# Kernel tuning notes

Measured on AMD Instinct MI355X. Metric: run time of the kernel, lower is better.

Reference implementation:

```python
import jax, jax.numpy as jnp
import numpy as np

HID = 1024; INTER = 2048; NSTATE = 16; KCONV = 4; DTRANK = 64
NHEADS = 16; NKV = 4; HDIM = 64; VHDIM = 128; EPS = 1e-6
ATTN_H = HID; K_H = NKV * HDIM; V_H = NKV * VHDIM
LATENT = INTER + ATTN_H + K_H + V_H  # 3840


def rmsnorm(x, w, eps=EPS):
    return x * jax.lax.rsqrt(jnp.mean(x * x, axis=-1, keepdims=True) + eps) * w


def setup_inputs():
    key = jax.random.key(0)
    ks = jax.random.split(key, 8)
    B, S = 2, 2048
    s = 0.02
    x = jax.random.normal(ks[0], (B, S, HID), jnp.float32)
    W_in = jax.random.normal(ks[1], (LATENT + INTER, HID), jnp.float32) * s
    conv_w = jax.random.normal(ks[2], (INTER, KCONV), jnp.float32) * 0.2
    conv_b = jnp.zeros((INTER,), jnp.float32)
    W_x = jax.random.normal(ks[3], (DTRANK + 2 * NSTATE, INTER), jnp.float32) * s
    dt_ln_w = jnp.ones((DTRANK,), jnp.float32)
    B_ln_w = jnp.ones((NSTATE,), jnp.float32)
    C_ln_w = jnp.ones((NSTATE,), jnp.float32)
    W_dt = jax.random.normal(ks[4], (INTER, DTRANK), jnp.float32) * s
    b_dt = jnp.log(jnp.expm1(jnp.full((INTER,), 0.01, jnp.float32)))
    A_log = jnp.log(jnp.broadcast_to(jnp.arange(1, NSTATE + 1, dtype=jnp.float32)[None, :], (INTER, NSTATE)))
    D_param = jnp.ones((INTER,), jnp.float32)
    ln1_w = jnp.ones((INTER,), jnp.float32)
    ln2_w = jnp.ones((INTER,), jnp.float32)
    W_out = jax.random.normal(ks[5], (HID, INTER), jnp.float32) * s
    return {"x": x, "W_in": W_in, "conv_w": conv_w, "conv_b": conv_b, "W_x": W_x,
            "dt_ln_w": dt_ln_w, "B_ln_w": B_ln_w, "C_ln_w": C_ln_w, "W_dt": W_dt,
            "b_dt": b_dt, "A_log": A_log, "D_param": D_param, "ln1_w": ln1_w,
            "ln2_w": ln2_w, "W_out": W_out}


def reference(x, W_in, conv_w, conv_b, W_x, dt_ln_w, B_ln_w, C_ln_w, W_dt, b_dt,
              A_log, D_param, ln1_w, ln2_w, W_out):
    Bsz, S, _ = x.shape
    proj = x @ W_in.T  # [B,S,LATENT+INTER]
    q = proj[..., :ATTN_H]
    k = proj[..., ATTN_H:ATTN_H + K_H]
    v = proj[..., ATTN_H + K_H:ATTN_H + K_H + V_H]
    xs = proj[..., ATTN_H + K_H + V_H:LATENT]
    gate = proj[..., LATENT:]

    # depthwise causal conv1d + silu (causal_conv1d_fn)
    xt = xs.transpose(0, 2, 1)  # [B,D,S]
    xc = jax.lax.conv_general_dilated(xt, conv_w[:, None, :], (1,), [(KCONV - 1, 0)],
                                      feature_group_count=INTER,
                                      dimension_numbers=("NCH", "OIH", "NCH"))
    xc = jax.nn.silu(xc + conv_b[None, :, None]).transpose(0, 2, 1)  # [B,S,D]

    # input-dependent dt, B, C with inner RMSNorms
    ssm_p = xc @ W_x.T  # [B,S,DTRANK+2N]
    dt = rmsnorm(ssm_p[..., :DTRANK], dt_ln_w)
    Bm = rmsnorm(ssm_p[..., DTRANK:DTRANK + NSTATE], B_ln_w)
    Cm = rmsnorm(ssm_p[..., DTRANK + NSTATE:], C_ln_w)
    delta = jax.nn.softplus(dt @ W_dt.T + b_dt)  # [B,S,D] (delta_bias + softplus)
    A = -jnp.exp(A_log)  # [D,N]

    def step(h, inp):
        d_t, b_t, c_t, x_t = inp  # [B,D],[B,N],[B,N],[B,D]
        dA = jnp.exp(d_t[:, :, None] * A)  # [B,D,N]
        h = h * dA + (d_t * x_t)[:, :, None] * b_t[:, None, :]
        y = jnp.einsum("bdn,bn->bd", h, c_t)
        return h, y

    h0 = jnp.zeros((Bsz, INTER, NSTATE), x.dtype)
    _, ys = jax.lax.scan(step, h0, (delta.transpose(1, 0, 2), Bm.transpose(1, 0, 2),
                                    Cm.transpose(1, 0, 2), xc.transpose(1, 0, 2)))
    y = ys.transpose(1, 0, 2) + xc * D_param
    y = y * jax.nn.silu(gate)  # gated scan output [B,S,INTER]

    # causal GQA attention branch (no output proj; v_head_dim = INTER/NHEADS)
    qh = q.reshape(Bsz, S, NHEADS, HDIM).transpose(0, 2, 1, 3)
    kh = jnp.repeat(k.reshape(Bsz, S, NKV, HDIM), NHEADS // NKV, axis=2).transpose(0, 2, 1, 3)
    vh = jnp.repeat(v.reshape(Bsz, S, NKV, VHDIM), NHEADS // NKV, axis=2).transpose(0, 2, 1, 3)
    scores = jnp.einsum("bhqd,bhkd->bhqk", qh, kh) * (1.0 / float(np.sqrt(HDIM)))
    mask = jnp.tril(jnp.ones((S, S), bool))
    scores = jnp.where(mask, scores, jnp.finfo(scores.dtype).min)
    attn = jnp.einsum("bhqk,bhkd->bhqd", jax.nn.softmax(scores, axis=-1), vh)
    attn = attn.transpose(0, 2, 1, 3).reshape(Bsz, S, INTER)

    out = (rmsnorm(attn, ln1_w) + rmsnorm(y, ln2_w)) * 0.5
    return out @ W_out.T
```

## Files before the change

### kernel.cpp

```cpp
#include <hip/hip_runtime.h>
#include <stdint.h>

#define HID    1024
#define INTER  2048
#define NSTATE 16
#define DTRANK 64
#define NHEADS 16
#define NKV    4
#define HDIM   64
#define VHDIM  128
#define ATTN_H 1024
#define K_H    256
#define V_H    512
#define LATENT 3840
#define NCOLS  5888
#define BATCH  2
#define SEQ    2048
#define T_TOT  4096
#define NCHUNK 64
#define CHLEN  32
#define LOG2E  1.44269504f

typedef __bf16 bf16x8 __attribute__((ext_vector_type(8)));
typedef float  f32x4  __attribute__((ext_vector_type(4)));
typedef float  f32x4v __attribute__((ext_vector_type(4)));
typedef unsigned short u16x8 __attribute__((ext_vector_type(8)));

__device__ __forceinline__ float bf2f(unsigned short u) {
    return __uint_as_float(((unsigned int)u) << 16);
}
__device__ __forceinline__ unsigned short f2bf(float f) {
    unsigned int u = __float_as_uint(f);
    u = (u + 0x7fffu + ((u >> 16) & 1u)) >> 16;
    return (unsigned short)u;
}
__device__ __forceinline__ bf16x8 ldb8(const unsigned short* p) {
    return __builtin_bit_cast(bf16x8, *(const u16x8*)p);
}

typedef const __attribute__((address_space(1))) unsigned int* gas_ptr;
typedef __attribute__((address_space(3))) unsigned int* las_ptr;
__device__ __forceinline__ void load_lds16(const void* g, void* l) {
    __builtin_amdgcn_global_load_lds((gas_ptr)g, (las_ptr)l, 16, 0, 0);
}

__global__ void k_prep(const float* __restrict__ x, const float* __restrict__ W_in,
                       const float* __restrict__ W_dt, const float* __restrict__ W_out,
                       const float* __restrict__ W_x,
                       unsigned short* __restrict__ xbf, unsigned short* __restrict__ Winbf,
                       unsigned short* __restrict__ Wdtbf, unsigned short* __restrict__ Woutbf,
                       unsigned short* __restrict__ Wxpad) {
    int i = blockIdx.x * 256 + threadIdx.x;
    const float* src; unsigned short* dst; int off;
    if (i < 524288)        { src = x;     dst = xbf;    off = i; }
    else if (i < 1277952)  { src = W_in;  dst = Winbf;  off = i - 524288; }
    else if (i < 1294336)  { src = W_dt;  dst = Wdtbf;  off = i - 1277952; }
    else if (i < 1556480)  { src = W_out; dst = Woutbf; off = i - 1294336; }
    else {
        int e = (i - 1556480) * 8;
        int row = e >> 11, col = e & 2047;
        u16x8 o;
        if (row < DTRANK + 2 * NSTATE) {
#pragma unroll
            for (int k = 0; k < 8; k++) o[k] = f2bf(W_x[(size_t)row * INTER + col + k]);
        } else {
#pragma unroll
            for (int k = 0; k < 8; k++) o[k] = 0;
        }
        *(u16x8*)(Wxpad + e) = o;
        return;
    }
    f32x4v a = ((const f32x4v*)src)[2 * off];
    f32x4v b = ((const f32x4v*)src)[2 * off + 1];
    u16x8 o;
#pragma unroll
    for (int k = 0; k < 4; k++) { o[k] = f2bf(a[k]); o[k + 4] = f2bf(b[k]); }
    *(u16x8*)(dst + (size_t)off * 8) = o;
}

template <int NT>
__launch_bounds__(512)
__global__ void k_gemm8(const unsigned short* __restrict__ A, const unsigned short* __restrict__ B,
                        unsigned short* __restrict__ C, int lda, int ldb, int ldc) {
    __shared__ __align__(16) unsigned short As[3][256 * 64];
    __shared__ __align__(16) unsigned short Bs[3][128 * 64];
    const int tid = threadIdx.x;
    const int lane = tid & 63;
    const int w = tid >> 6;
    const int wm = w >> 1, wn = w & 1;
    const int l15 = lane & 15, hi = lane >> 4;
    const int nwg = gridDim.x * gridDim.y;
    int lin = blockIdx.y * gridDim.x + blockIdx.x;
    lin = (lin & 7) * (nwg >> 3) + (lin >> 3);
    const int bm = (lin / gridDim.x) * 256;
    const int bn = (lin % gridDim.x) * 128;

    const int srcCol = ((lane & 7) ^ (lane >> 3)) * 8;

    auto stageA = [&](int buf, int kt, int u) {
        int rsb = 64 * u + 8 * w;
        load_lds16(A + (size_t)(bm + rsb + (lane >> 3)) * lda + kt * 64 + srcCol, &As[buf][rsb * 64]);
    };
    auto stageB = [&](int buf, int kt, int u) {
        int rsb = 64 * u + 8 * w;
        load_lds16(B + (size_t)(bn + rsb + (lane >> 3)) * ldb + kt * 64 + srcCol, &Bs[buf][rsb * 64]);
    };

    f32x4 acc[4][4];
#pragma unroll
    for (int i = 0; i < 4; i++)
#pragma unroll
        for (int j = 0; j < 4; j++) acc[i][j] = (f32x4){0.f, 0.f, 0.f, 0.f};

    auto phase = [&](int buf, int kk, auto stageThunk, int vm) {
        bf16x8 a_[4], b_[4];
        const int cc = (kk << 2) + hi;
#pragma unroll
        for (int mi = 0; mi < 4; ++mi) {
            int row = 64 * wm + 16 * mi + l15;
            a_[mi] = ldb8(&As[buf][row * 64 + ((cc ^ (row & 7)) << 3)]);
        }
#pragma unroll
        for (int ni = 0; ni < 4; ++ni) {
            int row = 64 * wn + 16 * ni + l15;
            b_[ni] = ldb8(&Bs[buf][row * 64 + ((cc ^ (row & 7)) << 3)]);
        }
        stageThunk();
        if (vm == 1)      asm volatile("s_waitcnt vmcnt(6)" ::: "memory");
        else if (vm == 2) asm volatile("s_waitcnt vmcnt(0)" ::: "memory");
        __builtin_amdgcn_s_barrier();
        __builtin_amdgcn_s_setprio(1);
#pragma unroll
        for (int mi = 0; mi < 4; ++mi)
#pragma unroll
            for (int ni = 0; ni < 4; ++ni)
                acc[mi][ni] = __builtin_amdgcn_mfma_f32_16x16x32_bf16(a_[mi], b_[ni], acc[mi][ni], 0, 0, 0);
        __builtin_amdgcn_s_setprio(0);
        __builtin_amdgcn_s_barrier();
    };

#pragma unroll
    for (int u = 0; u < 4; ++u) stageA(0, 0, u);
    stageB(0, 0, 0); stageB(0, 0, 1);
#pragma unroll
    for (int u = 0; u < 4; ++u) stageA(1, 1, u);
    stageB(1, 1, 0); stageB(1, 1, 1);
    asm volatile("s_waitcnt vmcnt(6)" ::: "memory");
    __builtin_amdgcn_s_barrier();

    int buf = 0;
    for (int t = 0; t < NT; ++t) {
        const int kt = t + 2;
        const bool st = kt < NT;
        const int pbuf = (buf + 2 >= 3) ? buf - 1 : buf + 2;
        phase(buf, 0, [&] {
            if (st) { stageA(pbuf, kt, 0); stageA(pbuf, kt, 1); stageA(pbuf, kt, 2); }
        }, 0);
        phase(buf, 1, [&] {
            if (st) { stageA(pbuf, kt, 3); stageB(pbuf, kt, 0); stageB(pbuf, kt, 1); }
        }, st ? 1 : 2);
        buf = (buf + 1 >= 3) ? 0 : buf + 1;
    }

#pragma unroll
    for (int mi = 0; mi < 4; ++mi)
#pragma unroll
        for (int ni = 0; ni < 4; ++ni)
#pragma unroll
            for (int r = 0; r < 4; ++r) {
                int grow = bm + 64 * wm + 16 * mi + (hi << 2) + r;
                int gcol = bn + 64 * wn + 16 * ni + l15;
                C[(size_t)grow * ldc + gcol] = f2bf(acc[mi][ni][r]);
            }
}

template <int OUT_MODE>
__launch_bounds__(256)
__global__ void k_gemm(const unsigned short* __restrict__ A, const unsigned short* __restrict__ B,
                       void* __restrict__ Cout, const float* __restrict__ bias,
                       int M, int N, int K, int lda, int ldb, int ldc) {
    __shared__ __align__(16) unsigned short As[128 * 64];
    __shared__ __align__(16) unsigned short Bs[128 * 64];
    const int tid = threadIdx.x;
    const int lane = tid & 63;
    const int w = tid >> 6;
    const int wm = w >> 1, wn = w & 1;
    const int nwg = gridDim.x * gridDim.y;
    int lin = blockIdx.y * gridDim.x + blockIdx.x;
    lin = (lin & 7) * (nwg >> 3) + (lin >> 3);
    const int bm = (lin / gridDim.x) * 128, bn = (lin % gridDim.x) * 128;
    const size_t koff = (OUT_MODE == 3) ? (size_t)blockIdx.z * K : 0;

    f32x4 acc[4][4];
#pragma unroll
    for (int i = 0; i < 4; i++)
#pragma unroll
        for (int j = 0; j < 4; j++) acc[i][j] = (f32x4){0.f, 0.f, 0.f, 0.f};

    const int nk = K >> 6;
    for (int ks = 0; ks < nk; ++ks) {
        const int k0 = ks << 6;
#pragma unroll
        for (int i = 0; i < 4; ++i) {
            int qb = (w << 6) + (i << 8);
            int q = qb + lane;
            int row = q >> 3, c = q & 7;
            int csrc = c ^ (row & 7);
            load_lds16(A + (size_t)(bm + row) * lda + koff + k0 + csrc * 8, As + qb * 8);
            load_lds16(B + (size_t)(bn + row) * ldb + koff + k0 + csrc * 8, Bs + qb * 8);
        }
        __syncthreads();
#pragma unroll
        for (int kk = 0; kk < 2; ++kk) {
            bf16x8 af[4], bfr[4];
#pragma unroll
            for (int mi = 0; mi < 4; mi++) {
                int row = (wm << 6) + (mi << 4) + (lane & 15);
                int c = (kk << 2) + (lane >> 4);
                af[mi] = ldb8(As + row * 64 + (c ^ (row & 7)) * 8);
            }
#pragma unroll
            for (int ni = 0; ni < 4; ni++) {
                int row = (wn << 6) + (ni << 4) + (lane & 15);
                int c = (kk << 2) + (lane >> 4);
                bfr[ni] = ldb8(Bs + row * 64 + (c ^ (row & 7)) * 8);
            }
#pragma unroll
            for (int mi = 0; mi < 4; mi++)
#pragma unroll
                for (int ni = 0; ni < 4; ni++)
                    acc[mi][ni] = __builtin_amdgcn_mfma_f32_16x16x32_bf16(af[mi], bfr[ni], acc[mi][ni], 0, 0, 0);
        }
        __syncthreads();
    }
#pragma unroll
    for (int mi = 0; mi < 4; mi++)
#pragma unroll
        for (int ni = 0; ni < 4; ni++)
#pragma unroll
            for (int r = 0; r < 4; r++) {
                int grow = bm + (wm << 6) + (mi << 4) + ((lane >> 4) << 2) + r;
                int gcol = bn + (wn << 6) + (ni << 4) + (lane & 15);
                float v = acc[mi][ni][r];
                if (OUT_MODE == 0) {
                    ((unsigned short*)Cout)[(size_t)grow * ldc + gcol] = f2bf(v);
                } else if (OUT_MODE == 1) {
                    ((float*)Cout)[(size_t)grow * ldc + gcol] = v;
                } else if (OUT_MODE == 3) {
                    ((float*)Cout)[(size_t)blockIdx.z * M * ldc + (size_t)grow * ldc + gcol] = v;
                } else {
                    v += bias[gcol];
                    v = (v > 20.f) ? v : log1pf(__expf(v));
                    ((unsigned short*)Cout)[(size_t)grow * ldc + gcol] = f2bf(v);
                }
            }
}

__global__ void k_conv(const unsigned short* __restrict__ proj, const float* __restrict__ conv_w,
                       const float* __restrict__ conv_b, unsigned short* __restrict__ xc) {
    int r = blockIdx.x;
    int d8 = threadIdx.x * 8;
    int t = r & (SEQ - 1);
    float accv[8];
#pragma unroll
    for (int i = 0; i < 8; i++) accv[i] = conv_b[d8 + i];
#pragma unroll
    for (int j = 0; j < 4; j++) {
        int tp = t - 3 + j;
        if (tp < 0) continue;
        u16x8 xv = *(const u16x8*)(proj + (size_t)(r - 3 + j) * NCOLS + (LATENT - INTER) + d8);
#pragma unroll
        for (int i = 0; i < 8; i++) accv[i] += conv_w[(d8 + i) * 4 + j] * bf2f(xv[i]);
    }
    u16x8 o;
#pragma unroll
    for (int i = 0; i < 8; i++) {
        float v = accv[i];
        v = v / (1.f + __expf(-v));
        o[i] = f2bf(v);
    }
    *(u16x8*)(xc + (size_t)r * INTER + d8) = o;
}

__global__ void k_rms3(const float* __restrict__ ssmp, const float* __restrict__ dt_w,
                       const float* __restrict__ B_w, const float* __restrict__ C_w,
                       unsigned short* __restrict__ dtbf, float* __restrict__ Bm, float* __restrict__ Cm) {
    int r = blockIdx.x;
    int tid = threadIdx.x;
    int lane = tid & 63, w = tid >> 6;
    int c = tid;
    float v = 0.f;
    if (c < 96) {
#pragma unroll
        for (int s = 0; s < 8; s++) v += ssmp[(size_t)s * (T_TOT * 128) + (size_t)r * 128 + c];
    }
    float s = v * v;
    if (w == 0) {
#pragma unroll
        for (int d = 1; d < 64; d <<= 1) s += __shfl_xor(s, d);
        float rms = rsqrtf(s * (1.f / 64.f) + 1e-6f);
        dtbf[(size_t)r * 64 + lane] = f2bf(v * rms * dt_w[lane]);
    } else {
#pragma unroll
        for (int d = 1; d < 16; d <<= 1) s += __shfl_xor(s, d);
        float rms = rsqrtf(s * (1.f / 16.f) + 1e-6f);
        if (lane < 16) Bm[(size_t)r * 16 + lane] = v * rms * B_w[lane];
        else if (lane < 32) Cm[(size_t)r * 16 + (lane - 16)] = v * rms * C_w[lane - 16];
    }
}

template <int PASS>
__launch_bounds__(256)
__global__ void k_scan_chunk(const unsigned short* __restrict__ deltabf, const unsigned short* __restrict__ xcbf,
                             const float* __restrict__ Bm, const float* __restrict__ Cm,
                             const float* __restrict__ A_log,
                             float* __restrict__ hend, float* __restrict__ sumd,
                             const float* __restrict__ hinit, unsigned short* __restrict__ ybf) {
    __shared__ __align__(16) unsigned short dltS[CHLEN * 256];
    __shared__ __align__(16) unsigned short xvS[CHLEN * 256];
    __shared__ __align__(16) float BsT[CHLEN * 16];
    __shared__ __align__(16) float CsT[CHLEN * 16];
    const int d0 = blockIdx.x * 256;
    const int c = blockIdx.y;
    const int b = blockIdx.z;
    const int tid = threadIdx.x, lane = tid & 63, w = tid >> 6;
    const int t0 = c * CHLEN;
    const size_t rowbase = (size_t)(b * SEQ + t0);

    float An[16];
    {
        const f32x4* ap = (const f32x4*)(A_log + (size_t)(d0 + tid) * 16);
#pragma unroll
        for (int n4 = 0; n4 < 4; n4++) {
            f32x4 av = ap[n4];
#pragma unroll
            for (int j = 0; j < 4; j++) An[n4 * 4 + j] = -LOG2E * __expf(av[j]);
        }
    }

#pragma unroll
    for (int i = 0; i < 4; ++i) {
        int qb = (w << 6) + (i << 8);
        int q = qb + lane;
        int t = q >> 5, coff = q & 31;
        load_lds16(deltabf + (rowbase + t) * INTER + d0 + coff * 8, dltS + qb * 8);
        load_lds16(xcbf + (rowbase + t) * INTER + d0 + coff * 8, xvS + qb * 8);
    }
    if (tid < 128) {
        ((f32x4*)BsT)[tid] = ((const f32x4*)(Bm + rowbase * 16))[tid];
        if (PASS == 2) ((f32x4*)CsT)[tid] = ((const f32x4*)(Cm + rowbase * 16))[tid];
    }
    __syncthreads();

    const size_t sidx = ((size_t)(c * BATCH + b) * INTER + d0 + tid) * 16;
    float h[16];
    if (PASS == 2) {
        const f32x4* hp = (const f32x4*)(hinit + sidx);
#pragma unroll
        for (int n4 = 0; n4 < 4; n4++) {
            f32x4 hv = hp[n4];
#pragma unroll
            for (int j = 0; j < 4; j++) h[n4 * 4 + j] = hv[j];
        }
    } else {
#pragma unroll
        for (int n = 0; n < 16; n++) h[n] = 0.f;
    }
    float sd = 0.f;
    for (int t = 0; t < CHLEN; ++t) {
        float dlt = bf2f(dltS[t * 256 + tid]);
        float xv = bf2f(xvS[t * 256 + tid]);
        float dx = dlt * xv;
        if (PASS == 0) sd += dlt;
        float y = 0.f;
#pragma unroll
        for (int n4 = 0; n4 < 4; ++n4) {
            f32x4 Bt = ((f32x4*)BsT)[t * 4 + n4];
            f32x4 Ct;
            if (PASS == 2) Ct = ((f32x4*)CsT)[t * 4 + n4];
#pragma unroll
            for (int j = 0; j < 4; ++j) {
                int n = n4 * 4 + j;
                float a = exp2f(dlt * An[n]);
                h[n] = h[n] * a + dx * Bt[j];
                if (PASS == 2) y += h[n] * Ct[j];
            }
        }
        if (PASS == 2) ybf[(rowbase + t) * INTER + d0 + tid] = f2bf(y);
    }
    if (PASS == 0) {
        f32x4* hp = (f32x4*)(hend + sidx);
#pragma unroll
        for (int n4 = 0; n4 < 4; n4++) {
            f32x4 hv;
#pragma unroll
            for (int j = 0; j < 4; j++) hv[j] = h[n4 * 4 + j];
            hp[n4] = hv;
        }
        sumd[(size_t)(c * BATCH + b) * INTER + d0 + tid] = sd;
    }
}

__global__ void k_scan_prop(const float* __restrict__ A_log, const float* __restrict__ hend,
                            const float* __restrict__ sumd, float* __restrict__ hinit) {
    const int tid = blockIdx.x * 256 + threadIdx.x;
    const int n = tid & 15;
    const int d = (tid >> 4) & (INTER - 1);
    const float An = -LOG2E * __expf(A_log[(size_t)d * 16 + n]);
    const int bd = tid >> 4;
    float h = 0.f;
#pragma unroll 1
    for (int cb = 0; cb < NCHUNK / 4; ++cb) {
        float he[4], sdv[4];
#pragma unroll
        for (int j = 0; j < 4; j++) {
            int c = cb * 4 + j;
            he[j] = hend[(size_t)c * 65536 + tid];
            sdv[j] = sumd[(size_t)c * 4096 + bd];
        }
#pragma unroll
        for (int j = 0; j < 4; j++) {
            int c = cb * 4 + j;
            hinit[(size_t)c * 65536 + tid] = h;
            h = he[j] + exp2f(An * sdv[j]) * h;
        }
    }
}

__launch_bounds__(256)
__global__ void k_attn(const unsigned short* __restrict__ proj, unsigned short* __restrict__ attn) {
    __shared__ __align__(16) unsigned short Ks[64 * 64];
    __shared__ __align__(16) unsigned short Vt[128 * 64];
    __shared__ __align__(16) unsigned short Ps[4 * 16 * 64];
    const int pair = blockIdx.x;
    const int h = blockIdx.y;
    const int b = blockIdx.z;
    const int g = h >> 2;
    const int tid = threadIdx.x, lane = tid & 63, w = tid >> 6;
    const int l15 = lane & 15, hi = lane >> 4;

    const int krow = tid >> 3, kc = tid & 7;
    const int kp2 = (tid & 31) * 2, vb = tid >> 5;

    const unsigned short* kbase = proj + (size_t)(b * SEQ) * NCOLS + ATTN_H + g * HDIM;
    const unsigned short* vbase = proj + (size_t)(b * SEQ) * NCOLS + (ATTN_H + K_H) + g * VHDIM;

    u16x8 krA[2], vrA[2][2], krB[2], vrB[2][2];

    auto LOAD = [&](u16x8* kr, u16x8 (*vr)[2], int kv) {
        const unsigned short* kp_ = kbase + (size_t)(kv + krow) * NCOLS + kc * 8;
        kr[0] = *(const u16x8*)kp_;
        kr[1] = *(const u16x8*)(kp_ + (size_t)32 * NCOLS);
        const unsigned short* vp_ = vbase + (size_t)(kv + kp2) * NCOLS + vb * 8;
        vr[0][0] = *(const u16x8*)vp_;
        vr[0][1] = *(const u16x8*)(vp_ + NCOLS);
        vr[1][0] = *(const u16x8*)(vp_ + 64);
        vr[1][1] = *(const u16x8*)(vp_ + NCOLS + 64);
    };
    auto WRITE = [&](u16x8* kr, u16x8 (*vr)[2]) {
        int ksw = (kc ^ (krow & 7)) << 3;
        *(u16x8*)&Ks[krow * 64 + ksw] = kr[0];
        *(u16x8*)&Ks[(krow + 32) * 64 + ksw] = kr[1];
#pragma unroll
        for (int hf = 0; hf < 2; hf++) {
            u16x8 va = vr[hf][0], vb2 = vr[hf][1];
#pragma unroll
            for (int i = 0; i < 8; i++) {
                unsigned int pk = (unsigned int)va[i] | ((unsigned int)vb2[i] << 16);
                int r = (vb + hf * 8) * 8 + i;
                *(unsigned int*)&Vt[r * 64 + (((kp2 >> 3) ^ (r & 7)) << 3) + (kp2 & 7)] = pk;
            }
        }
    };

    const float SC = 0.18033688f;

    for (int phase = 0; phase < 2; ++phase) {
        const int qt = (phase == 0) ? (31 - pair) : pair;
        const int qw = qt * 64 + w * 16;
        const int ntiles = qt + 1;

        bf16x8 qf[2];
        {
            int qr = qw + l15;
            const unsigned short* qp = proj + (size_t)(b * SEQ + qr) * NCOLS + h * HDIM + hi * 8;
            qf[0] = ldb8(qp);
            qf[1] = ldb8(qp + 32);
        }
        f32x4 O[8];
#pragma unroll
        for (int vf = 0; vf < 8; vf++) O[vf] = (f32x4){0.f, 0.f, 0.f, 0.f};
        float l_[4] = {0.f, 0.f, 0.f, 0.f};

        auto COMPUTE = [&](int kv, bool MASK) {
            const int pbase = w * 1024;
            f32x4 sv[4];
#pragma unroll
            for (int cf = 0; cf < 4; ++cf) {
                f32x4 s = (f32x4){0.f, 0.f, 0.f, 0.f};
                int row = cf * 16 + l15;
#pragma unroll
                for (int kk = 0; kk < 2; ++kk) {
                    bf16x8 kb = ldb8(&Ks[row * 64 + ((((kk << 2) + hi) ^ (row & 7)) << 3)]);
                    s = __builtin_amdgcn_mfma_f32_16x16x32_bf16(qf[kk], kb, s, 0, 0, 0);
                }
                sv[cf] = s;
            }
            const int qi0 = qw + (hi << 2);
#pragma unroll
            for (int cf = 0; cf < 4; ++cf) {
                int ki = kv + cf * 16 + l15;
#pragma unroll
                for (int rg = 0; rg < 4; ++rg) {
                    float v;
                    if (MASK) v = (ki <= qi0 + rg) ? exp2f(sv[cf][rg] * SC) : 0.f;
                    else      v = exp2f(sv[cf][rg] * SC);
                    l_[rg] += v;
                    int pr = (hi << 2) + rg;
                    int pc = cf * 16 + l15;
                    Ps[pbase + pr * 64 + (((pc >> 3) ^ (pr & 7)) << 3) + (pc & 7)] = f2bf(v);
                }
            }
            bf16x8 pa0 = ldb8(&Ps[pbase + l15 * 64 + ((hi ^ (l15 & 7)) << 3)]);
            bf16x8 pa1 = ldb8(&Ps[pbase + l15 * 64 + (((4 + hi) ^ (l15 & 7)) << 3)]);
#pragma unroll
            for (int vf = 0; vf < 8; ++vf) {
                int vr_ = vf * 16 + l15;
                bf16x8 v0 = ldb8(&Vt[vr_ * 64 + ((hi ^ (vr_ & 7)) << 3)]);
                bf16x8 v1 = ldb8(&Vt[vr_ * 64 + (((4 + hi) ^ (vr_ & 7)) << 3)]);
                O[vf] = __builtin_amdgcn_mfma_f32_16x16x32_bf16(pa0, v0, O[vf], 0, 0, 0);
                O[vf] = __builtin_amdgcn_mfma_f32_16x16x32_bf16(pa1, v1, O[vf], 0, 0, 0);
            }
        };

        LOAD(krA, vrA, 0);
        bool useA = true;
        for (int j = 0; j < ntiles; ++j) {
            if (useA) {
                WRITE(krA, vrA);
                if (j + 1 < ntiles) LOAD(krB, vrB, (j + 1) * 64);
            } else {
                WRITE(krB, vrB);
                if (j + 1 < ntiles) LOAD(krA, vrA, (j + 1) * 64);
            }
            __syncthreads();
            COMPUTE(j * 64, j == ntiles - 1);
            __syncthreads();
            useA = !useA;
        }

#pragma unroll
        for (int dd = 1; dd < 16; dd <<= 1)
#pragma unroll
            for (int rg = 0; rg < 4; ++rg) l_[rg] += __shfl_xor(l_[rg], dd);
#pragma unroll
        for (int rg = 0; rg < 4; ++rg) {
            float inv = 1.f / l_[rg];
            int grow = b * SEQ + qw + (hi << 2) + rg;
#pragma unroll
            for (int vf = 0; vf < 8; ++vf) {
                int gcol = h * VHDIM + vf * 16 + l15;
                attn[(size_t)grow * INTER + gcol] = f2bf(O[vf][rg] * inv);
            }
        }
    }
}

__launch_bounds__(256)
__global__ void k_fuse(const unsigned short* __restrict__ attn, const unsigned short* __restrict__ ybf,
                       const unsigned short* __restrict__ xc, const unsigned short* __restrict__ proj,
                       const float* __restrict__ Dp, const float* __restrict__ ln1,
                       const float* __restrict__ ln2, unsigned short* __restrict__ fused) {
    __shared__ float red[8];
    int r = blockIdx.x, tid = threadIdx.x;
    int c8 = tid * 8;
    u16x8 av = *(const u16x8*)(attn + (size_t)r * INTER + c8);
    u16x8 yv8 = *(const u16x8*)(ybf + (size_t)r * INTER + c8);
    u16x8 xv8 = *(const u16x8*)(xc + (size_t)r * INTER + c8);
    u16x8 gv8 = *(const u16x8*)(proj + (size_t)r * NCOLS + LATENT + c8);
    float a_[8], y_[8];
    float ssa = 0.f, ssy = 0.f;
#pragma unroll
    for (int i = 0; i < 8; i++) {
        float a = bf2f(av[i]);
        float yv = bf2f(yv8[i]) + bf2f(xv8[i]) * Dp[c8 + i];
        float gg = bf2f(gv8[i]);
        yv *= gg / (1.f + __expf(-gg));
        a_[i] = a; y_[i] = yv;
        ssa += a * a; ssy += yv * yv;
    }
#pragma unroll
    for (int d = 1; d < 64; d <<= 1) { ssa += __shfl_xor(ssa, d); ssy += __shfl_xor(ssy, d); }
    int w = tid >> 6, lane = tid & 63;
    if (lane == 0) { red[w * 2] = ssa; red[w * 2 + 1] = ssy; }
    __syncthreads();
    ssa = red[0] + red[2] + red[4] + red[6];
    ssy = red[1] + red[3] + red[5] + red[7];
    float ra = rsqrtf(ssa * (1.f / 2048.f) + 1e-6f);
    float ry = rsqrtf(ssy * (1.f / 2048.f) + 1e-6f);
    u16x8 o;
#pragma unroll
    for (int i = 0; i < 8; i++) {
        float v = (a_[i] * ra * ln1[c8 + i] + y_[i] * ry * ln2[c8 + i]) * 0.5f;
        o[i] = f2bf(v);
    }
    *(u16x8*)(fused + (size_t)r * INTER + c8) = o;
}

extern "C" void kernel_launch(void* const* d_in, const int* in_sizes, int n_in,
                              void* d_out, int out_size, void* d_ws, size_t ws_size,
                              hipStream_t stream) {
    const float* x      = (const float*)d_in[0];
    const float* W_in   = (const float*)d_in[1];
    const float* conv_w = (const float*)d_in[2];
    const float* conv_b = (const float*)d_in[3];
    const float* W_x    = (const float*)d_in[4];
    const float* dt_w   = (const float*)d_in[5];
    const float* B_w    = (const float*)d_in[6];
    const float* C_w    = (const float*)d_in[7];
    const float* W_dt   = (const float*)d_in[8];
    const float* b_dt   = (const float*)d_in[9];
    const float* A_log  = (const float*)d_in[10];
    const float* Dp     = (const float*)d_in[11];
    const float* ln1    = (const float*)d_in[12];
    const float* ln2    = (const float*)d_in[13];
    const float* W_out  = (const float*)d_in[14];
    float* out = (float*)d_out;

    char* p = (char*)d_ws;
    auto alloc = [&](size_t bytes) -> void* {
        void* r = (void*)p;
        p += (bytes + 255) & ~(size_t)255;
        return r;
    };
    unsigned short* xbf     = (unsigned short*)alloc((size_t)T_TOT * HID * 2);
    unsigned short* Winbf   = (unsigned short*)alloc((size_t)NCOLS * HID * 2);
    unsigned short* projbf  = (unsigned short*)alloc((size_t)T_TOT * NCOLS * 2);
    unsigned short* xcbf    = (unsigned short*)alloc((size_t)T_TOT * INTER * 2);
    unsigned short* Wxpad   = (unsigned short*)alloc((size_t)128 * INTER * 2);
    float*          ssmp    = (float*)alloc((size_t)8 * T_TOT * 128 * 4);
    unsigned short* dtbf    = (unsigned short*)alloc((size_t)T_TOT * DTRANK * 2);
    float*          Bm      = (float*)alloc((size_t)T_TOT * 16 * 4);
    float*          Cm      = (float*)alloc((size_t)T_TOT * 16 * 4);
    unsigned short* Wdtbf   = (unsigned short*)alloc((size_t)INTER * DTRANK * 2);
    unsigned short* deltabf = (unsigned short*)alloc((size_t)T_TOT * INTER * 2);
    unsigned short* ybf     = (unsigned short*)alloc((size_t)T_TOT * INTER * 2);
    unsigned short* attnbf  = (unsigned short*)alloc((size_t)T_TOT * INTER * 2);
    unsigned short* fusedbf = (unsigned short*)alloc((size_t)T_TOT * INTER * 2);
    unsigned short* Woutbf  = (unsigned short*)alloc((size_t)HID * INTER * 2);
    float*          hendws  = (float*)alloc((size_t)NCHUNK * BATCH * INTER * 16 * 4);
    float*          hinitws = (float*)alloc((size_t)NCHUNK * BATCH * INTER * 16 * 4);
    float*          sumdws  = (float*)alloc((size_t)NCHUNK * BATCH * INTER * 4);

    k_prep<<<6208, 256, 0, stream>>>(x, W_in, W_dt, W_out, W_x, xbf, Winbf, Wdtbf, Woutbf, Wxpad);

    k_gemm8<16><<<dim3(NCOLS / 128, T_TOT / 256), 512, 0, stream>>>(
        xbf, Winbf, projbf, HID, HID, NCOLS);
    k_conv<<<T_TOT, 256, 0, stream>>>(projbf, conv_w, conv_b, xcbf);
    k_gemm<3><<<dim3(1, T_TOT / 128, 8), 256, 0, stream>>>(
        xcbf, Wxpad, ssmp, nullptr, T_TOT, 128, 256, INTER, INTER, 128);
    k_rms3<<<T_TOT, 128, 0, stream>>>(ssmp, dt_w, B_w, C_w, dtbf, Bm, Cm);
    k_gemm<2><<<dim3(INTER / 128, T_TOT / 128), 256, 0, stream>>>(
        dtbf, Wdtbf, deltabf, b_dt, T_TOT, INTER, DTRANK, DTRANK, DTRANK, INTER);
    k_scan_chunk<0><<<dim3(INTER / 256, NCHUNK, BATCH), 256, 0, stream>>>(
        deltabf, xcbf, Bm, Cm, A_log, hendws, sumdws, nullptr, nullptr);
    k_scan_prop<<<256, 256, 0, stream>>>(A_log, hendws, sumdws, hinitws);
    k_scan_chunk<2><<<dim3(INTER / 256, NCHUNK, BATCH), 256, 0, stream>>>(
        deltabf, xcbf, Bm, Cm, A_log, nullptr, nullptr, hinitws, ybf);
    k_attn<<<dim3(16, NHEADS, BATCH), 256, 0, stream>>>(projbf, attnbf);
    k_fuse<<<T_TOT, 256, 0, stream>>>(attnbf, ybf, xcbf, projbf, Dp, ln1, ln2, fusedbf);
    k_gemm<1><<<dim3(HID / 128, T_TOT / 128), 256, 0, stream>>>(
        fusedbf, Woutbf, out, nullptr, T_TOT, HID, INTER, INTER, INTER, HID);
}
```

Before: 407.8 us.

## Split attention KV tiles across two blocks and split-K the output GEMM

The attention kernel now runs twice as many blocks. Each block handles every other KV tile and writes unnormalized bf16 partial outputs plus per-row partial softmax sums. The fuse kernel combines the two partials and normalizes them before the RMS norms. The output projection GEMM is also split along K into two fp32 partial buffers, summed by a new elementwise add kernel. The goal is to raise the block count so all CUs stay busy on the attention and final GEMM, at the cost of extra global traffic for the partial buffers and one more kernel launch.

```diff
diff --git a/kernel.cpp b/kernel.cpp
--- a/kernel.cpp
+++ b/kernel.cpp
@@ -256,6 +256,13 @@
             }
 }
 
+__global__ void k_addout(const float* __restrict__ part, float* __restrict__ out) {
+    int i = blockIdx.x * 256 + threadIdx.x;
+    f32x4 a = ((const f32x4*)part)[i];
+    f32x4 b = ((const f32x4*)(part + (size_t)T_TOT * HID))[i];
+    ((f32x4*)out)[i] = a + b;
+}
+
 __global__ void k_conv(const unsigned short* __restrict__ proj, const float* __restrict__ conv_w,
                        const float* __restrict__ conv_b, unsigned short* __restrict__ xc) {
     int r = blockIdx.x;
@@ -428,13 +435,15 @@
 }
 
 __launch_bounds__(256)
-__global__ void k_attn(const unsigned short* __restrict__ proj, unsigned short* __restrict__ attn) {
+__global__ void k_attn(const unsigned short* __restrict__ proj, unsigned short* __restrict__ attnp,
+                       float* __restrict__ lsum) {
     __shared__ __align__(16) unsigned short Ks[64 * 64];
     __shared__ __align__(16) unsigned short Vt[128 * 64];
     __shared__ __align__(16) unsigned short Ps[4 * 16 * 64];
     const int pair = blockIdx.x;
     const int h = blockIdx.y;
-    const int b = blockIdx.z;
+    const int b = blockIdx.z >> 1;
+    const int half = blockIdx.z & 1;
     const int g = h >> 2;
     const int tid = threadIdx.x, lane = tid & 63, w = tid >> 6;
     const int l15 = lane & 15, hi = lane >> 4;
@@ -478,7 +487,7 @@
     for (int phase = 0; phase < 2; ++phase) {
         const int qt = (phase == 0) ? (31 - pair) : pair;
         const int qw = qt * 64 + w * 16;
-        const int ntiles = qt + 1;
+        const int nt2 = (qt >= half) ? (((qt - half) >> 1) + 1) : 0;
 
         bf16x8 qf[2];
         {
@@ -533,48 +542,56 @@
             }
         };
 
-        LOAD(krA, vrA, 0);
-        bool useA = true;
-        for (int j = 0; j < ntiles; ++j) {
-            if (useA) {
-                WRITE(krA, vrA);
-                if (j + 1 < ntiles) LOAD(krB, vrB, (j + 1) * 64);
-            } else {
-                WRITE(krB, vrB);
-                if (j + 1 < ntiles) LOAD(krA, vrA, (j + 1) * 64);
-            }
-            __syncthreads();
-            COMPUTE(j * 64, j == ntiles - 1);
-            __syncthreads();
-            useA = !useA;
+        if (nt2 > 0) {
+            LOAD(krA, vrA, half * 64);
+            bool useA = true;
+            for (int jj = 0; jj < nt2; ++jj) {
+                int j = half + 2 * jj;
+                if (useA) {
+                    WRITE(krA, vrA);
+                    if (jj + 1 < nt2) LOAD(krB, vrB, (j + 2) * 64);
+                } else {
+                    WRITE(krB, vrB);
+                    if (jj + 1 < nt2) LOAD(krA, vrA, (j + 2) * 64);
+                }
+                __syncthreads();
+                COMPUTE(j * 64, j == qt);
+                __syncthreads();
+                useA = !useA;
+            }
         }
 
 #pragma unroll
         for (int dd = 1; dd < 16; dd <<= 1)
 #pragma unroll
             for (int rg = 0; rg < 4; ++rg) l_[rg] += __shfl_xor(l_[rg], dd);
+        const size_t obase = (size_t)half * T_TOT * INTER;
 #pragma unroll
         for (int rg = 0; rg < 4; ++rg) {
-            float inv = 1.f / l_[rg];
             int grow = b * SEQ + qw + (hi << 2) + rg;
+            if (l15 == 0) lsum[(size_t)half * T_TOT * 16 + (size_t)grow * 16 + h] = l_[rg];
 #pragma unroll
             for (int vf = 0; vf < 8; ++vf) {
                 int gcol = h * VHDIM + vf * 16 + l15;
-                attn[(size_t)grow * INTER + gcol] = f2bf(O[vf][rg] * inv);
+                attnp[obase + (size_t)grow * INTER + gcol] = f2bf(O[vf][rg]);
             }
         }
     }
 }
 
 __launch_bounds__(256)
-__global__ void k_fuse(const unsigned short* __restrict__ attn, const unsigned short* __restrict__ ybf,
+__global__ void k_fuse(const unsigned short* __restrict__ attnp, const float* __restrict__ lsum,
+                       const unsigned short* __restrict__ ybf,
                        const unsigned short* __restrict__ xc, const unsigned short* __restrict__ proj,
                        const float* __restrict__ Dp, const float* __restrict__ ln1,
                        const float* __restrict__ ln2, unsigned short* __restrict__ fused) {
     __shared__ float red[8];
     int r = blockIdx.x, tid = threadIdx.x;
     int c8 = tid * 8;
-    u16x8 av = *(const u16x8*)(attn + (size_t)r * INTER + c8);
+    int hh = tid >> 4;
+    u16x8 av0 = *(const u16x8*)(attnp + (size_t)r * INTER + c8);
+    u16x8 av1 = *(const u16x8*)(attnp + (size_t)T_TOT * INTER + (size_t)r * INTER + c8);
+    float linv = 1.f / (lsum[(size_t)r * 16 + hh] + lsum[(size_t)T_TOT * 16 + (size_t)r * 16 + hh]);
     u16x8 yv8 = *(const u16x8*)(ybf + (size_t)r * INTER + c8);
     u16x8 xv8 = *(const u16x8*)(xc + (size_t)r * INTER + c8);
     u16x8 gv8 = *(const u16x8*)(proj + (size_t)r * NCOLS + LATENT + c8);
@@ -582,7 +599,7 @@
     float ssa = 0.f, ssy = 0.f;
 #pragma unroll
     for (int i = 0; i < 8; i++) {
-        float a = bf2f(av[i]);
+        float a = (bf2f(av0[i]) + bf2f(av1[i])) * linv;
         float yv = bf2f(yv8[i]) + bf2f(xv8[i]) * Dp[c8 + i];
         float gg = bf2f(gv8[i]);
         yv *= gg / (1.f + __expf(-gg));
@@ -645,12 +662,14 @@
     unsigned short* Wdtbf   = (unsigned short*)alloc((size_t)INTER * DTRANK * 2);
     unsigned short* deltabf = (unsigned short*)alloc((size_t)T_TOT * INTER * 2);
     unsigned short* ybf     = (unsigned short*)alloc((size_t)T_TOT * INTER * 2);
-    unsigned short* attnbf  = (unsigned short*)alloc((size_t)T_TOT * INTER * 2);
+    unsigned short* attnp   = (unsigned short*)alloc((size_t)2 * T_TOT * INTER * 2);
+    float*          lsum    = (float*)alloc((size_t)2 * T_TOT * 16 * 4);
     unsigned short* fusedbf = (unsigned short*)alloc((size_t)T_TOT * INTER * 2);
     unsigned short* Woutbf  = (unsigned short*)alloc((size_t)HID * INTER * 2);
     float*          hendws  = (float*)alloc((size_t)NCHUNK * BATCH * INTER * 16 * 4);
     float*          hinitws = (float*)alloc((size_t)NCHUNK * BATCH * INTER * 16 * 4);
     float*          sumdws  = (float*)alloc((size_t)NCHUNK * BATCH * INTER * 4);
+    float*          outpart = (float*)alloc((size_t)2 * T_TOT * HID * 4);
 
     k_prep<<<6208, 256, 0, stream>>>(x, W_in, W_dt, W_out, W_x, xbf, Winbf, Wdtbf, Woutbf, Wxpad);
 
@@ -667,8 +686,9 @@
     k_scan_prop<<<256, 256, 0, stream>>>(A_log, hendws, sumdws, hinitws);
     k_scan_chunk<2><<<dim3(INTER / 256, NCHUNK, BATCH), 256, 0, stream>>>(
         deltabf, xcbf, Bm, Cm, A_log, nullptr, nullptr, hinitws, ybf);
-    k_attn<<<dim3(16, NHEADS, BATCH), 256, 0, stream>>>(projbf, attnbf);
-    k_fuse<<<T_TOT, 256, 0, stream>>>(attnbf, ybf, xcbf, projbf, Dp, ln1, ln2, fusedbf);
-    k_gemm<1><<<dim3(HID / 128, T_TOT / 128), 256, 0, stream>>>(
-        fusedbf, Woutbf, out, nullptr, T_TOT, HID, INTER, INTER, INTER, HID);
-}
+    k_attn<<<dim3(16, NHEADS, BATCH * 2), 256, 0, stream>>>(projbf, attnp, lsum);
+    k_fuse<<<T_TOT, 256, 0, stream>>>(attnp, lsum, ybf, xcbf, projbf, Dp, ln1, ln2, fusedbf);
+    k_gemm<3><<<dim3(HID / 128, T_TOT / 128, 2), 256, 0, stream>>>(
+        fusedbf, Woutbf, outpart, nullptr, T_TOT, HID, 1024, INTER, INTER, HID);
+    k_addout<<<T_TOT * HID / 1024, 256, 0, stream>>>(outpart, out);
+}
```

Measured after the change: 422.6 us. 3.6% more time.

## Double-buffer attention K/V in LDS, add MFMA priority, split-K output GEMM

Applied to the files above, without the earlier changes.

The attention kernel now keeps two LDS buffers for K and V. The next tile's global loads are issued before the current tile's compute and written to LDS afterwards, so each iteration needs one barrier instead of two. s_setprio is raised around the MFMA sections. Separately, the final output GEMM is split along K into two partial fp32 buffers and summed by a new elementwise kernel. This doubles the block count of that GEMM at the cost of extra memory traffic and one more launch.

```diff
diff --git a/kernel.cpp b/kernel.cpp
--- a/kernel.cpp
+++ b/kernel.cpp
@@ -256,6 +256,13 @@
             }
 }
 
+__global__ void k_addout(const float* __restrict__ part, float* __restrict__ out) {
+    int i = blockIdx.x * 256 + threadIdx.x;
+    f32x4 a = ((const f32x4*)part)[i];
+    f32x4 b = ((const f32x4*)(part + (size_t)T_TOT * HID))[i];
+    ((f32x4*)out)[i] = a + b;
+}
+
 __global__ void k_conv(const unsigned short* __restrict__ proj, const float* __restrict__ conv_w,
                        const float* __restrict__ conv_b, unsigned short* __restrict__ xc) {
     int r = blockIdx.x;
@@ -429,8 +436,8 @@
 
 __launch_bounds__(256)
 __global__ void k_attn(const unsigned short* __restrict__ proj, unsigned short* __restrict__ attn) {
-    __shared__ __align__(16) unsigned short Ks[64 * 64];
-    __shared__ __align__(16) unsigned short Vt[128 * 64];
+    __shared__ __align__(16) unsigned short Ks[2][64 * 64];
+    __shared__ __align__(16) unsigned short Vt[2][128 * 64];
     __shared__ __align__(16) unsigned short Ps[4 * 16 * 64];
     const int pair = blockIdx.x;
     const int h = blockIdx.y;
@@ -445,9 +452,9 @@
     const unsigned short* kbase = proj + (size_t)(b * SEQ) * NCOLS + ATTN_H + g * HDIM;
     const unsigned short* vbase = proj + (size_t)(b * SEQ) * NCOLS + (ATTN_H + K_H) + g * VHDIM;
 
-    u16x8 krA[2], vrA[2][2], krB[2], vrB[2][2];
-
-    auto LOAD = [&](u16x8* kr, u16x8 (*vr)[2], int kv) {
+    u16x8 kr[2], vr[2][2];
+
+    auto LOAD = [&](int kv) {
         const unsigned short* kp_ = kbase + (size_t)(kv + krow) * NCOLS + kc * 8;
         kr[0] = *(const u16x8*)kp_;
         kr[1] = *(const u16x8*)(kp_ + (size_t)32 * NCOLS);
@@ -457,10 +464,10 @@
         vr[1][0] = *(const u16x8*)(vp_ + 64);
         vr[1][1] = *(const u16x8*)(vp_ + NCOLS + 64);
     };
-    auto WRITE = [&](u16x8* kr, u16x8 (*vr)[2]) {
+    auto WRITE = [&](int nb) {
         int ksw = (kc ^ (krow & 7)) << 3;
-        *(u16x8*)&Ks[krow * 64 + ksw] = kr[0];
-        *(u16x8*)&Ks[(krow + 32) * 64 + ksw] = kr[1];
+        *(u16x8*)&Ks[nb][krow * 64 + ksw] = kr[0];
+        *(u16x8*)&Ks[nb][(krow + 32) * 64 + ksw] = kr[1];
 #pragma unroll
         for (int hf = 0; hf < 2; hf++) {
             u16x8 va = vr[hf][0], vb2 = vr[hf][1];
@@ -468,7 +475,7 @@
             for (int i = 0; i < 8; i++) {
                 unsigned int pk = (unsigned int)va[i] | ((unsigned int)vb2[i] << 16);
                 int r = (vb + hf * 8) * 8 + i;
-                *(unsigned int*)&Vt[r * 64 + (((kp2 >> 3) ^ (r & 7)) << 3) + (kp2 & 7)] = pk;
+                *(unsigned int*)&Vt[nb][r * 64 + (((kp2 >> 3) ^ (r & 7)) << 3) + (kp2 & 7)] = pk;
             }
         }
     };
@@ -492,20 +499,22 @@
         for (int vf = 0; vf < 8; vf++) O[vf] = (f32x4){0.f, 0.f, 0.f, 0.f};
         float l_[4] = {0.f, 0.f, 0.f, 0.f};
 
-        auto COMPUTE = [&](int kv, bool MASK) {
+        auto COMPUTE = [&](int kv, bool MASK, int cb) {
             const int pbase = w * 1024;
             f32x4 sv[4];
+            __builtin_amdgcn_s_setprio(1);
 #pragma unroll
             for (int cf = 0; cf < 4; ++cf) {
                 f32x4 s = (f32x4){0.f, 0.f, 0.f, 0.f};
                 int row = cf * 16 + l15;
 #pragma unroll
                 for (int kk = 0; kk < 2; ++kk) {
-                    bf16x8 kb = ldb8(&Ks[row * 64 + ((((kk << 2) + hi) ^ (row & 7)) << 3)]);
+                    bf16x8 kb = ldb8(&Ks[cb][row * 64 + ((((kk << 2) + hi) ^ (row & 7)) << 3)]);
                     s = __builtin_amdgcn_mfma_f32_16x16x32_bf16(qf[kk], kb, s, 0, 0, 0);
                 }
                 sv[cf] = s;
             }
+            __builtin_amdgcn_s_setprio(0);
             const int qi0 = qw + (hi << 2);
 #pragma unroll
             for (int cf = 0; cf < 4; ++cf) {
@@ -523,30 +532,26 @@
             }
             bf16x8 pa0 = ldb8(&Ps[pbase + l15 * 64 + ((hi ^ (l15 & 7)) << 3)]);
             bf16x8 pa1 = ldb8(&Ps[pbase + l15 * 64 + (((4 + hi) ^ (l15 & 7)) << 3)]);
+            __builtin_amdgcn_s_setprio(1);
 #pragma unroll
             for (int vf = 0; vf < 8; ++vf) {
                 int vr_ = vf * 16 + l15;
-                bf16x8 v0 = ldb8(&Vt[vr_ * 64 + ((hi ^ (vr_ & 7)) << 3)]);
-                bf16x8 v1 = ldb8(&Vt[vr_ * 64 + (((4 + hi) ^ (vr_ & 7)) << 3)]);
+                bf16x8 v0 = ldb8(&Vt[cb][vr_ * 64 + ((hi ^ (vr_ & 7)) << 3)]);
+                bf16x8 v1 = ldb8(&Vt[cb][vr_ * 64 + (((4 + hi) ^ (vr_ & 7)) << 3)]);
                 O[vf] = __builtin_amdgcn_mfma_f32_16x16x32_bf16(pa0, v0, O[vf], 0, 0, 0);
                 O[vf] = __builtin_amdgcn_mfma_f32_16x16x32_bf16(pa1, v1, O[vf], 0, 0, 0);
             }
+            __builtin_amdgcn_s_setprio(0);
         };
 
-        LOAD(krA, vrA, 0);
-        bool useA = true;
+        LOAD(0);
+        WRITE(0);
+        __syncthreads();
         for (int j = 0; j < ntiles; ++j) {
-            if (useA) {
-                WRITE(krA, vrA);
-                if (j + 1 < ntiles) LOAD(krB, vrB, (j + 1) * 64);
-            } else {
-                WRITE(krB, vrB);
-                if (j + 1 < ntiles) LOAD(krA, vrA, (j + 1) * 64);
-            }
+            if (j + 1 < ntiles) LOAD((j + 1) * 64);
+            COMPUTE(j * 64, j == ntiles - 1, j & 1);
+            if (j + 1 < ntiles) WRITE((j + 1) & 1);
             __syncthreads();
-            COMPUTE(j * 64, j == ntiles - 1);
-            __syncthreads();
-            useA = !useA;
         }
 
 #pragma unroll
@@ -651,6 +656,7 @@
     float*          hendws  = (float*)alloc((size_t)NCHUNK * BATCH * INTER * 16 * 4);
     float*          hinitws = (float*)alloc((size_t)NCHUNK * BATCH * INTER * 16 * 4);
     float*          sumdws  = (float*)alloc((size_t)NCHUNK * BATCH * INTER * 4);
+    float*          outpart = (float*)alloc((size_t)2 * T_TOT * HID * 4);
 
     k_prep<<<6208, 256, 0, stream>>>(x, W_in, W_dt, W_out, W_x, xbf, Winbf, Wdtbf, Woutbf, Wxpad);
 
@@ -669,6 +675,7 @@
         deltabf, xcbf, Bm, Cm, A_log, nullptr, nullptr, hinitws, ybf);
     k_attn<<<dim3(16, NHEADS, BATCH), 256, 0, stream>>>(projbf, attnbf);
     k_fuse<<<T_TOT, 256, 0, stream>>>(attnbf, ybf, xcbf, projbf, Dp, ln1, ln2, fusedbf);
-    k_gemm<1><<<dim3(HID / 128, T_TOT / 128), 256, 0, stream>>>(
-        fusedbf, Woutbf, out, nullptr, T_TOT, HID, INTER, INTER, INTER, HID);
-}
+    k_gemm<3><<<dim3(HID / 128, T_TOT / 128, 2), 256, 0, stream>>>(
+        fusedbf, Woutbf, outpart, nullptr, T_TOT, HID, 1024, INTER, INTER, HID);
+    k_addout<<<T_TOT * HID / 1024, 256, 0, stream>>>(outpart, out);
+}
```

Result: no change. 407.4 us (-0.1%).
